# Optimization experiments

Measured on AMD Instinct MI355X. Metric: run time of the kernel, lower is better.

## Reference

```python
import jax, jax.numpy as jnp
import numpy as np

EMB = 512
HEADS = 16
WS = 8          # window size
B = 8
HW = 64         # height = width = sqrt(num_tokens)
N = HW * HW
E_HEAD = EMB // HEADS
WN = HW // WS   # windows per side
SHIFT = WS // 2

# --- static index/mask tables (numpy, baked at trace time) ---
_idx = np.array([[x, y] for x in range(WS) for y in range(WS)])
_REL = _idx[None, :, :] - _idx[:, None, :] + WS - 1   # [WS^2, WS^2, 2]

def _shift_masks():
    m = np.zeros((WS * WS, WS * WS), dtype=np.float32)
    s = WS * (WS // 2)
    m[-s:, :-s] = -np.inf
    m[:-s, -s:] = -np.inf
    r = (WS * WS) // WS
    # einops '(r w1) (c w2) -> (w1 r) (w2 c)'
    col = m.reshape(r, WS, r, WS).transpose(1, 0, 3, 2).reshape(WS * WS, WS * WS)
    return jnp.asarray(m), jnp.asarray(col)

_ROW_MASK, _COL_MASK = _shift_masks()

def _window(x):
    # x: [B, HW, HW, EMB]; channel split '(e H)' -> e outer, H inner
    x = x.reshape(B, WN, WS, WN, WS, E_HEAD, HEADS)
    x = x.transpose(0, 6, 1, 3, 2, 4, 5)            # b H Wh Ww w1 w2 e
    return x.reshape(B, HEADS, WN, WN, WS * WS, E_HEAD)

def _unwindow(x):
    # 'b H Wh Ww (w1 w2) e -> b (Wh w1) (Ww w2) (H e)'
    x = x.reshape(B, HEADS, WN, WN, WS, WS, E_HEAD)
    x = x.transpose(0, 2, 4, 3, 5, 1, 6)
    return x.reshape(B, HW, HW, EMB).reshape(B, N, EMB)

def _forward(content, style, scale, shift,
             W1, b1, W2, b2, Wsc, bsc, Wsh, bsh,
             Wso, bso, Wsho, bsho, pos_emb):
    c = content @ W1.T + b1
    s = style   @ W2.T + b2
    sc = scale  @ Wsc.T + bsc
    sh = shift  @ Wsh.T + bsh
    # to spatial grid and shifted roll (no inverse roll in original code)
    def grid(x):
        x = x.reshape(B, HW, HW, EMB)
        return jnp.roll(x, (-SHIFT, -SHIFT), axis=(1, 2))
    Q  = _window(grid(c))
    K  = _window(grid(s))
    Vs = _window(grid(sc))
    Vh = _window(grid(sh))
    inv_sqrt = 1.0 / np.sqrt(EMB / HEADS)
    wei = jnp.einsum('bhijqe,bhijke->bhijqk', Q, K) * inv_sqrt
    wei = wei + pos_emb[_REL[:, :, 0], _REL[:, :, 1]]
    wei = wei.at[:, :, -1, :].add(_ROW_MASK)
    wei = wei.at[:, :, :, -1].add(_COL_MASK)
    w = jax.nn.softmax(wei, axis=-1)
    out_sc = _unwindow(jnp.einsum('bhijqk,bhijke->bhijqe', w, Vs))
    out_sh = _unwindow(jnp.einsum('bhijqk,bhijke->bhijqe', w, Vh))
    return out_sc @ Wso.T + bso, out_sh @ Wsho.T + bsho

def setup_inputs() -> dict:
    key = jax.random.key(0)
    ks = jax.random.split(key, 18)
    def lin(i):
        return (0.02 * jax.random.normal(ks[i], (EMB, EMB), jnp.float32),
                jnp.zeros((EMB,), jnp.float32))
    W1, b1 = lin(0); W2, b2 = lin(1); Wsc, bsc = lin(2); Wsh, bsh = lin(3)
    Wso, bso = lin(4); Wsho, bsho = lin(5)
    return {
        'content': jax.random.normal(ks[6], (B, N, EMB), jnp.float32),
        'style':   jax.random.normal(ks[7], (B, N, EMB), jnp.float32),
        'scale':   jax.random.normal(ks[8], (B, N, EMB), jnp.float32),
        'shift':   jax.random.normal(ks[9], (B, N, EMB), jnp.float32),
        'W1': W1, 'b1': b1, 'W2': W2, 'b2': b2,
        'Wsc': Wsc, 'bsc': bsc, 'Wsh': Wsh, 'bsh': bsh,
        'Wso': Wso, 'bso': bso, 'Wsho': Wsho, 'bsho': bsho,
        'pos_emb': jax.random.normal(ks[10], (2 * WS - 1, 2 * WS - 1), jnp.float32),
    }

def reference(content, style, scale, shift, W1, b1, W2, b2, Wsc, bsc, Wsh, bsh,
              Wso, bso, Wsho, bsho, pos_emb):
    return _forward(content, style, scale, shift, W1, b1, W2, b2,
                    Wsc, bsc, Wsh, bsh, Wso, bso, Wsho, bsho, pos_emb)
```

## Files before the change

### kernel.cpp

```cpp
#include <hip/hip_runtime.h>
#include <hip/hip_bf16.h>
#include <math.h>

#define EMB 512
#define HEADS 16
#define WS 8
#define BSZ 8
#define HW 64
#define NTOK (HW * HW)
#define WN 8
#define M_TOT (BSZ * NTOK)
#define NELEM ((size_t)M_TOT * EMB)

typedef _Float16 f16;
typedef _Float16 f16x4 __attribute__((ext_vector_type(4)));
typedef _Float16 f16x8 __attribute__((ext_vector_type(8)));
typedef float f32x4 __attribute__((ext_vector_type(4)));

struct CvtW { const float* w[6]; const float* b[4]; f16* out[6]; float* bp; };

__global__ __launch_bounds__(128) void cvt_w(CvtW P) {
  const int z = blockIdx.y;
  const int np = blockIdx.x;
  const int src = (z < 4) ? ((np & 31) * 16 + (np >> 5)) : np;
  const float4* __restrict__ in = (const float4*)(P.w[z] + (size_t)src * 512);
  f16x4* __restrict__ out = (f16x4*)(P.out[z] + (size_t)np * 512);
  const int t = threadIdx.x;
  float4 v = in[t];
  f16x4 h = {(f16)v.x, (f16)v.y, (f16)v.z, (f16)v.w};
  out[t] = h;
  if (t == 0 && z < 4) P.bp[z * 512 + np] = P.b[z][src];
}

struct GemmF16 { const void* X[4]; const f16* W[4]; const float* Bi[4]; void* O[4]; };

template <bool CVT_A, typename OutT>
__global__ __launch_bounds__(256) void gemm_mfma(GemmF16 P) {
  const int z = blockIdx.z;
  const f16* __restrict__ B = P.W[z];
  const float* __restrict__ Bi = P.Bi[z];
  OutT* __restrict__ O = (OutT*)P.O[z];

  __shared__ f16 lds[2][2][128 * 32];

  const int tid = threadIdx.x;
  const int lane = tid & 63;
  const int wid = tid >> 6;
  const int wr = wid >> 1, wc = wid & 1;
  const size_t m0 = (size_t)blockIdx.x * 128;
  const size_t n0 = (size_t)blockIdx.y * 128;

  const f16*  Ag16 = CVT_A ? (const f16*)nullptr : ((const f16*)P.X[z] + m0 * 512);
  const float* Ag32 = CVT_A ? ((const float*)P.X[z] + m0 * 512) : (const float*)nullptr;
  const f16* Bg = B + n0 * 512;

  const int rl = lane >> 2;
  const int qs = (lane & 3) ^ ((rl >> 1) & 3);
  const size_t goff16 = (size_t)rl * 512 + (size_t)qs * 8;

  const int c = lane & 15;
  const int g = lane >> 4;

  int aoff[4], boff[4];
  #pragma unroll
  for (int i = 0; i < 4; ++i) {
    const int rowa = wr * 64 + i * 16 + c;
    aoff[i] = rowa * 32 + ((g ^ ((rowa >> 1) & 3)) * 8);
    const int rowb = wc * 64 + i * 16 + c;
    boff[i] = rowb * 32 + ((g ^ ((rowb >> 1) & 3)) * 8);
  }

  f32x4 acc[4][4];
  #pragma unroll
  for (int i = 0; i < 4; ++i)
    #pragma unroll
    for (int j = 0; j < 4; ++j) acc[i][j] = (f32x4){0.f, 0.f, 0.f, 0.f};

  float4 areg[2][2];

#define LOAD_A32(k0) do { if (CVT_A) {                                         \
    _Pragma("unroll")                                                          \
    for (int ii = 0; ii < 2; ++ii) {                                           \
      const int s = wid * 2 + ii;                                              \
      const float* ga = Ag32 + (size_t)(s * 16 + rl) * 512 + (size_t)(k0)      \
                        + (size_t)qs * 8;                                      \
      areg[ii][0] = *(const float4*)ga;                                        \
      areg[ii][1] = *(const float4*)(ga + 4);                                  \
    } } } while (0)

#define WRITE_A(buf) do { if (CVT_A) {                                         \
    _Pragma("unroll")                                                          \
    for (int ii = 0; ii < 2; ++ii) {                                           \
      const int s = wid * 2 + ii;                                              \
      const float* ap = (const float*)&areg[ii][0];                            \
      f16x8 hv;                                                                \
      _Pragma("unroll")                                                        \
      for (int j = 0; j < 8; ++j) hv[j] = (f16)ap[j];                          \
      *(f16x8*)&lds[buf][0][(size_t)s * 512 + (size_t)lane * 8] = hv;          \
    } } } while (0)

#define STAGE_A16(buf, k0) do { if (!CVT_A) {                                  \
    _Pragma("unroll")                                                          \
    for (int ii = 0; ii < 2; ++ii) {                                           \
      const int s = wid * 2 + ii;                                              \
      const f16* ga = Ag16 + (size_t)s * 16 * 512 + (size_t)(k0) + goff16;     \
      __builtin_amdgcn_global_load_lds(                                        \
          (const __attribute__((address_space(1))) void*)ga,                   \
          (__attribute__((address_space(3))) void*)&lds[buf][0][s * 512],      \
          16, 0, 0);                                                           \
    } } } while (0)

#define STAGE_B(buf, k0) do {                                                  \
    _Pragma("unroll")                                                          \
    for (int ii = 0; ii < 2; ++ii) {                                           \
      const int s = wid * 2 + ii;                                              \
      const f16* gb = Bg + (size_t)s * 16 * 512 + (size_t)(k0) + goff16;       \
      __builtin_amdgcn_global_load_lds(                                        \
          (const __attribute__((address_space(1))) void*)gb,                   \
          (__attribute__((address_space(3))) void*)&lds[buf][1][s * 512],      \
          16, 0, 0);                                                           \
    } } while (0)

  LOAD_A32(0); STAGE_A16(0, 0); STAGE_B(0, 0); WRITE_A(0);
  __syncthreads();

  for (int t = 0; t < 16; ++t) {
    const int cur = t & 1;
    if (t < 15) { LOAD_A32((t + 1) * 32); STAGE_A16(cur ^ 1, (t + 1) * 32);
                  STAGE_B(cur ^ 1, (t + 1) * 32); }
    f16x8 af[4], bf[4];
    #pragma unroll
    for (int i = 0; i < 4; ++i) {
      af[i] = *(const f16x8*)&lds[cur][0][aoff[i]];
      bf[i] = *(const f16x8*)&lds[cur][1][boff[i]];
    }
    #pragma unroll
    for (int mi = 0; mi < 4; ++mi)
      #pragma unroll
      for (int ni = 0; ni < 4; ++ni)
        acc[mi][ni] = __builtin_amdgcn_mfma_f32_16x16x32_f16(
            af[mi], bf[ni], acc[mi][ni], 0, 0, 0);
    if (t < 15) WRITE_A(cur ^ 1);
    __syncthreads();
  }
#undef LOAD_A32
#undef WRITE_A
#undef STAGE_A16
#undef STAGE_B

  const int col_base = (int)n0 + wc * 64;
  const int row_base = (int)m0 + wr * 64 + g * 4;
  float bv[4];
  #pragma unroll
  for (int ni = 0; ni < 4; ++ni) bv[ni] = Bi[col_base + ni * 16 + c];
  #pragma unroll
  for (int mi = 0; mi < 4; ++mi)
    #pragma unroll
    for (int ni = 0; ni < 4; ++ni)
      #pragma unroll
      for (int r = 0; r < 4; ++r) {
        const size_t row = (size_t)(row_base + mi * 16 + r);
        O[row * 512 + col_base + ni * 16 + c] = (OutT)(acc[mi][ni][r] + bv[ni]);
      }
}

__global__ __launch_bounds__(256) void attn_kernel(
    const f16* __restrict__ cq, const f16* __restrict__ ck,
    const f16* __restrict__ vs, const f16* __restrict__ vh,
    const float* __restrict__ pe, f16* __restrict__ osc, f16* __restrict__ osh) {
  __shared__ f16 Pl[4][64][72];
  __shared__ float pesh[228];

  const int tid = threadIdx.x;
  for (int i = tid; i < 225; i += 256) pesh[i] = pe[i];
  __syncthreads();

  const int wid = tid >> 6;
  const int lane = tid & 63;
  const int g = lane >> 4;
  const int c = lane & 15;
  const int w = blockIdx.x * 4 + wid;
  const int wj = w & 7;
  const int wi = (w >> 3) & 7;
  const int h  = (w >> 6) & 15;
  const int b  = w >> 10;

  size_t taddr[4];
  #pragma unroll
  for (int i = 0; i < 4; ++i) {
    const int ty = (wi * 8 + i * 2 + (c >> 3) + 4) & 63;
    const int tx = (wj * 8 + (c & 7) + 4) & 63;
    taddr[i] = ((size_t)b * NTOK + ty * 64 + tx) * EMB + h * 32 + g * 8;
  }
  f16x8 kf[4], qf[4];
  #pragma unroll
  for (int i = 0; i < 4; ++i) {
    kf[i] = *(const f16x8*)(ck + taddr[i]);
    qf[i] = *(const f16x8*)(cq + taddr[i]);
  }

  f32x4 s[4][4];
  #pragma unroll
  for (int mt = 0; mt < 4; ++mt)
    #pragma unroll
    for (int kt = 0; kt < 4; ++kt) s[mt][kt] = (f32x4){0.f, 0.f, 0.f, 0.f};
  #pragma unroll
  for (int mt = 0; mt < 4; ++mt)
    #pragma unroll
    for (int kt = 0; kt < 4; ++kt)
      s[mt][kt] = __builtin_amdgcn_mfma_f32_16x16x32_f16(kf[mt], qf[kt],
                                                         s[mt][kt], 0, 0, 0);

  const float invs = 0.17677669529663687f;
  const bool rm = (wi == 7);
  const bool cm = (wj == 7) && (((c >> 2) & 1) != (g & 1));
  #pragma unroll
  for (int mt = 0; mt < 4; ++mt)
    #pragma unroll
    for (int kt = 0; kt < 4; ++kt) {
      const bool rmask = rm && ((mt >> 1) != (kt >> 1));
      const int ry = (mt - kt) * 2 + (g >> 1) - (c >> 3) + 7;
      #pragma unroll
      for (int r = 0; r < 4; ++r) {
        const int rx = (g & 1) * 4 + r - (c & 7) + 7;
        float d = s[mt][kt][r] * invs + pesh[ry * 15 + rx];
        if (rmask || cm) d = -1e30f;
        s[mt][kt][r] = d;
      }
    }

  #pragma unroll
  for (int kt = 0; kt < 4; ++kt) {
    float m = -1e30f;
    #pragma unroll
    for (int mt = 0; mt < 4; ++mt)
      #pragma unroll
      for (int r = 0; r < 4; ++r) m = fmaxf(m, s[mt][kt][r]);
    m = fmaxf(m, __shfl_xor(m, 16));
    m = fmaxf(m, __shfl_xor(m, 32));
    float sum = 0.f;
    #pragma unroll
    for (int mt = 0; mt < 4; ++mt)
      #pragma unroll
      for (int r = 0; r < 4; ++r) {
        const float p = __expf(s[mt][kt][r] - m);
        s[mt][kt][r] = p;
        sum += p;
      }
    sum += __shfl_xor(sum, 16);
    sum += __shfl_xor(sum, 32);
    const float rs = 1.f / sum;
    #pragma unroll
    for (int mt = 0; mt < 4; ++mt)
      #pragma unroll
      for (int r = 0; r < 4; ++r) s[mt][kt][r] *= rs;
  }

  #pragma unroll
  for (int mt = 0; mt < 4; ++mt)
    #pragma unroll
    for (int kt = 0; kt < 4; ++kt) {
      f16x4 pk = {(f16)s[mt][kt][0], (f16)s[mt][kt][1],
                  (f16)s[mt][kt][2], (f16)s[mt][kt][3]};
      *(f16x4*)&Pl[wid][kt * 16 + c][mt * 16 + g * 4] = pk;
    }

  size_t vb[2];
  #pragma unroll
  for (int ks = 0; ks < 2; ++ks) {
    const int vy = (wi * 8 + ks * 4 + g + 4) & 63;
    vb[ks] = ((size_t)b * NTOK + vy * 64) * EMB + h * 32 + c;
  }
  int xo[8];
  #pragma unroll
  for (int j = 0; j < 8; ++j) xo[j] = ((wj * 8 + j + 4) & 63) * EMB;

  f16x8 vfs[2][2], vfh[2][2];
  #pragma unroll
  for (int nt = 0; nt < 2; ++nt)
    #pragma unroll
    for (int ks = 0; ks < 2; ++ks)
      #pragma unroll
      for (int j = 0; j < 8; ++j) {
        const size_t a = vb[ks] + xo[j] + nt * 16;
        vfs[nt][ks][j] = vs[a];
        vfh[nt][ks][j] = vh[a];
      }

  f16x8 af[4][2];
  #pragma unroll
  for (int mt = 0; mt < 4; ++mt)
    #pragma unroll
    for (int ks = 0; ks < 2; ++ks)
      af[mt][ks] = *(const f16x8*)&Pl[wid][mt * 16 + c][ks * 32 + g * 8];

  size_t ob[4];
  #pragma unroll
  for (int mt = 0; mt < 4; ++mt) {
    const int np = (wi * 8 + 2 * mt + (g >> 1)) * 64 + wj * 8 + 4 * (g & 1);
    ob[mt] = ((size_t)b * NTOK + np) * EMB + h * 32 + c;
  }

  {
    f32x4 o[4][2];
    #pragma unroll
    for (int mt = 0; mt < 4; ++mt)
      #pragma unroll
      for (int nt = 0; nt < 2; ++nt) o[mt][nt] = (f32x4){0.f, 0.f, 0.f, 0.f};
    #pragma unroll
    for (int mt = 0; mt < 4; ++mt)
      #pragma unroll
      for (int nt = 0; nt < 2; ++nt)
        #pragma unroll
        for (int ks = 0; ks < 2; ++ks)
          o[mt][nt] = __builtin_amdgcn_mfma_f32_16x16x32_f16(
              af[mt][ks], vfs[nt][ks], o[mt][nt], 0, 0, 0);
    #pragma unroll
    for (int mt = 0; mt < 4; ++mt)
      #pragma unroll
      for (int nt = 0; nt < 2; ++nt)
        #pragma unroll
        for (int r = 0; r < 4; ++r)
          osc[ob[mt] + (size_t)r * EMB + nt * 16] = (f16)o[mt][nt][r];
  }
  {
    f32x4 o[4][2];
    #pragma unroll
    for (int mt = 0; mt < 4; ++mt)
      #pragma unroll
      for (int nt = 0; nt < 2; ++nt) o[mt][nt] = (f32x4){0.f, 0.f, 0.f, 0.f};
    #pragma unroll
    for (int mt = 0; mt < 4; ++mt)
      #pragma unroll
      for (int nt = 0; nt < 2; ++nt)
        #pragma unroll
        for (int ks = 0; ks < 2; ++ks)
          o[mt][nt] = __builtin_amdgcn_mfma_f32_16x16x32_f16(
              af[mt][ks], vfh[nt][ks], o[mt][nt], 0, 0, 0);
    #pragma unroll
    for (int mt = 0; mt < 4; ++mt)
      #pragma unroll
      for (int nt = 0; nt < 2; ++nt)
        #pragma unroll
        for (int r = 0; r < 4; ++r)
          osh[ob[mt] + (size_t)r * EMB + nt * 16] = (f16)o[mt][nt][r];
  }
}

extern "C" void kernel_launch(void* const* d_in, const int* in_sizes, int n_in,
                              void* d_out, int out_size, void* d_ws, size_t ws_size,
                              hipStream_t stream) {
  const float* content = (const float*)d_in[0];
  const float* style   = (const float*)d_in[1];
  const float* scalex  = (const float*)d_in[2];
  const float* shiftx  = (const float*)d_in[3];
  const float* W1  = (const float*)d_in[4];  const float* b1  = (const float*)d_in[5];
  const float* W2  = (const float*)d_in[6];  const float* b2  = (const float*)d_in[7];
  const float* Wsc = (const float*)d_in[8];  const float* bsc = (const float*)d_in[9];
  const float* Wsh = (const float*)d_in[10]; const float* bsh = (const float*)d_in[11];
  const float* Wso = (const float*)d_in[12]; const float* bso = (const float*)d_in[13];
  const float* Wsho= (const float*)d_in[14]; const float* bsho= (const float*)d_in[15];
  const float* pos = (const float*)d_in[16];
  float* out = (float*)d_out;

  f16* Wh = (f16*)d_ws;
  float* bp = (float*)(Wh + 6 * 262144);
  f16* Ph = (f16*)(bp + 2048);
  f16* Oh = Ph + 4 * NELEM;

  CvtW CW;
  CW.w[0] = W1; CW.w[1] = W2; CW.w[2] = Wsc; CW.w[3] = Wsh; CW.w[4] = Wso; CW.w[5] = Wsho;
  CW.b[0] = b1; CW.b[1] = b2; CW.b[2] = bsc; CW.b[3] = bsh;
  for (int i = 0; i < 6; ++i) CW.out[i] = Wh + (size_t)i * 262144;
  CW.bp = bp;
  hipLaunchKernelGGL(cvt_w, dim3(512, 6), dim3(128), 0, stream, CW);

  GemmF16 P1;
  P1.X[0] = content; P1.X[1] = style; P1.X[2] = scalex; P1.X[3] = shiftx;
  for (int i = 0; i < 4; ++i) {
    P1.W[i] = Wh + (size_t)i * 262144;
    P1.Bi[i] = bp + i * 512;
    P1.O[i] = Ph + (size_t)i * NELEM;
  }
  hipLaunchKernelGGL(HIP_KERNEL_NAME(gemm_mfma<true, f16>),
                     dim3(M_TOT / 128, EMB / 128, 4), dim3(256), 0, stream, P1);

  hipLaunchKernelGGL(attn_kernel, dim3(BSZ * HEADS * WN * WN / 4), dim3(256), 0,
                     stream, Ph, Ph + NELEM, Ph + 2 * NELEM, Ph + 3 * NELEM, pos,
                     Oh, Oh + NELEM);

  GemmF16 P2;
  P2.X[0] = Oh;          P2.W[0] = Wh + 4 * 262144; P2.Bi[0] = bso;  P2.O[0] = out;
  P2.X[1] = Oh + NELEM;  P2.W[1] = Wh + 5 * 262144; P2.Bi[1] = bsho; P2.O[1] = out + NELEM;
  P2.X[2] = P2.X[0]; P2.W[2] = P2.W[0]; P2.Bi[2] = P2.Bi[0]; P2.O[2] = P2.O[0];
  P2.X[3] = P2.X[1]; P2.W[3] = P2.W[1]; P2.Bi[3] = P2.Bi[1]; P2.O[3] = P2.O[1];
  hipLaunchKernelGGL(HIP_KERNEL_NAME(gemm_mfma<false, float>),
                     dim3(M_TOT / 128, EMB / 128, 2), dim3(256), 0, stream, P2);
}
```

Before: 523.7 us.

## Replace LDS-staged GEMM with direct global-to-register MFMA loads and 8 waves

The projection GEMMs no longer stage A and B tiles through shared memory. Each wave now loads its MFMA fragments straight from global memory into registers, using a two-slot register double buffer. Blocks grow to 512 threads (8 waves of 64x32 tiles), which removes the LDS traffic and the per-step barriers. In exchange there is no data sharing inside the block, so global and L2 traffic per block rises, and the per-lane loads are 16-32B strided reads across rows that may coalesce poorly.

```diff
diff --git a/kernel.cpp b/kernel.cpp
--- a/kernel.cpp
+++ b/kernel.cpp
@@ -35,132 +35,105 @@
 struct GemmF16 { const void* X[4]; const f16* W[4]; const float* Bi[4]; void* O[4]; };
 
 template <bool CVT_A, typename OutT>
-__global__ __launch_bounds__(256) void gemm_mfma(GemmF16 P) {
+__global__ __launch_bounds__(512) void gemm_direct(GemmF16 P) {
   const int z = blockIdx.z;
   const f16* __restrict__ B = P.W[z];
   const float* __restrict__ Bi = P.Bi[z];
   OutT* __restrict__ O = (OutT*)P.O[z];
-
-  __shared__ f16 lds[2][2][128 * 32];
+  const float* __restrict__ A32 = CVT_A ? (const float*)P.X[z] : (const float*)nullptr;
+  const f16*  __restrict__ A16 = CVT_A ? (const f16*)nullptr : (const f16*)P.X[z];
 
   const int tid = threadIdx.x;
   const int lane = tid & 63;
   const int wid = tid >> 6;
-  const int wr = wid >> 1, wc = wid & 1;
+  const int wr = wid >> 2;
+  const int wc = wid & 3;
+  const int g = lane >> 4;
+  const int c = lane & 15;
   const size_t m0 = (size_t)blockIdx.x * 128;
   const size_t n0 = (size_t)blockIdx.y * 128;
 
-  const f16*  Ag16 = CVT_A ? (const f16*)nullptr : ((const f16*)P.X[z] + m0 * 512);
-  const float* Ag32 = CVT_A ? ((const float*)P.X[z] + m0 * 512) : (const float*)nullptr;
-  const f16* Bg = B + n0 * 512;
-
-  const int rl = lane >> 2;
-  const int qs = (lane & 3) ^ ((rl >> 1) & 3);
-  const size_t goff16 = (size_t)rl * 512 + (size_t)qs * 8;
-
-  const int c = lane & 15;
-  const int g = lane >> 4;
-
-  int aoff[4], boff[4];
-  #pragma unroll
-  for (int i = 0; i < 4; ++i) {
-    const int rowa = wr * 64 + i * 16 + c;
-    aoff[i] = rowa * 32 + ((g ^ ((rowa >> 1) & 3)) * 8);
-    const int rowb = wc * 64 + i * 16 + c;
-    boff[i] = rowb * 32 + ((g ^ ((rowb >> 1) & 3)) * 8);
-  }
-
-  f32x4 acc[4][4];
-  #pragma unroll
-  for (int i = 0; i < 4; ++i)
-    #pragma unroll
-    for (int j = 0; j < 4; ++j) acc[i][j] = (f32x4){0.f, 0.f, 0.f, 0.f};
-
-  float4 areg[2][2];
-
-#define LOAD_A32(k0) do { if (CVT_A) {                                         \
+  size_t aoff[4], boff[2];
+  #pragma unroll
+  for (int mt = 0; mt < 4; ++mt)
+    aoff[mt] = (m0 + wr * 64 + mt * 16 + c) * 512 + g * 8;
+  #pragma unroll
+  for (int nt = 0; nt < 2; ++nt)
+    boff[nt] = ((size_t)n0 + wc * 32 + nt * 16 + c) * 512 + g * 8;
+
+  f32x4 acc[4][2];
+  #pragma unroll
+  for (int mt = 0; mt < 4; ++mt)
+    #pragma unroll
+    for (int nt = 0; nt < 2; ++nt) acc[mt][nt] = (f32x4){0.f, 0.f, 0.f, 0.f};
+
+  float4 alo0[4], ahi0[4], alo1[4], ahi1[4];
+  f16x8 a0[4], a1[4], b0[2], b1[2];
+
+#define LOADA(SLOT, K0) do {                                                   \
     _Pragma("unroll")                                                          \
-    for (int ii = 0; ii < 2; ++ii) {                                           \
-      const int s = wid * 2 + ii;                                              \
-      const float* ga = Ag32 + (size_t)(s * 16 + rl) * 512 + (size_t)(k0)      \
-                        + (size_t)qs * 8;                                      \
-      areg[ii][0] = *(const float4*)ga;                                        \
-      areg[ii][1] = *(const float4*)(ga + 4);                                  \
-    } } } while (0)
-
-#define WRITE_A(buf) do { if (CVT_A) {                                         \
+    for (int mt = 0; mt < 4; ++mt) {                                           \
+      if (CVT_A) {                                                             \
+        const float* p = A32 + aoff[mt] + (K0);                                \
+        alo##SLOT[mt] = *(const float4*)p;                                     \
+        ahi##SLOT[mt] = *(const float4*)(p + 4);                               \
+      } else {                                                                 \
+        a##SLOT[mt] = *(const f16x8*)(A16 + aoff[mt] + (K0));                  \
+      }                                                                        \
+    } } while (0)
+
+#define LOADB(SLOT, K0) do {                                                   \
     _Pragma("unroll")                                                          \
-    for (int ii = 0; ii < 2; ++ii) {                                           \
-      const int s = wid * 2 + ii;                                              \
-      const float* ap = (const float*)&areg[ii][0];                            \
-      f16x8 hv;                                                                \
+    for (int nt = 0; nt < 2; ++nt)                                             \
+      b##SLOT[nt] = *(const f16x8*)(B + boff[nt] + (K0));                      \
+  } while (0)
+
+#define COMPUTE(SLOT) do {                                                     \
+    f16x8 af[4];                                                               \
+    _Pragma("unroll")                                                          \
+    for (int mt = 0; mt < 4; ++mt) {                                           \
+      if (CVT_A) {                                                             \
+        const float4 u = alo##SLOT[mt], v = ahi##SLOT[mt];                     \
+        f16x8 hv = {(f16)u.x, (f16)u.y, (f16)u.z, (f16)u.w,                    \
+                    (f16)v.x, (f16)v.y, (f16)v.z, (f16)v.w};                   \
+        af[mt] = hv;                                                           \
+      } else {                                                                 \
+        af[mt] = a##SLOT[mt];                                                  \
+      }                                                                        \
+    }                                                                          \
+    _Pragma("unroll")                                                          \
+    for (int mt = 0; mt < 4; ++mt)                                             \
       _Pragma("unroll")                                                        \
-      for (int j = 0; j < 8; ++j) hv[j] = (f16)ap[j];                          \
-      *(f16x8*)&lds[buf][0][(size_t)s * 512 + (size_t)lane * 8] = hv;          \
-    } } } while (0)
-
-#define STAGE_A16(buf, k0) do { if (!CVT_A) {                                  \
-    _Pragma("unroll")                                                          \
-    for (int ii = 0; ii < 2; ++ii) {                                           \
-      const int s = wid * 2 + ii;                                              \
-      const f16* ga = Ag16 + (size_t)s * 16 * 512 + (size_t)(k0) + goff16;     \
-      __builtin_amdgcn_global_load_lds(                                        \
-          (const __attribute__((address_space(1))) void*)ga,                   \
-          (__attribute__((address_space(3))) void*)&lds[buf][0][s * 512],      \
-          16, 0, 0);                                                           \
-    } } } while (0)
-
-#define STAGE_B(buf, k0) do {                                                  \
-    _Pragma("unroll")                                                          \
-    for (int ii = 0; ii < 2; ++ii) {                                           \
-      const int s = wid * 2 + ii;                                              \
-      const f16* gb = Bg + (size_t)s * 16 * 512 + (size_t)(k0) + goff16;       \
-      __builtin_amdgcn_global_load_lds(                                        \
-          (const __attribute__((address_space(1))) void*)gb,                   \
-          (__attribute__((address_space(3))) void*)&lds[buf][1][s * 512],      \
-          16, 0, 0);                                                           \
-    } } while (0)
-
-  LOAD_A32(0); STAGE_A16(0, 0); STAGE_B(0, 0); WRITE_A(0);
-  __syncthreads();
-
-  for (int t = 0; t < 16; ++t) {
-    const int cur = t & 1;
-    if (t < 15) { LOAD_A32((t + 1) * 32); STAGE_A16(cur ^ 1, (t + 1) * 32);
-                  STAGE_B(cur ^ 1, (t + 1) * 32); }
-    f16x8 af[4], bf[4];
-    #pragma unroll
-    for (int i = 0; i < 4; ++i) {
-      af[i] = *(const f16x8*)&lds[cur][0][aoff[i]];
-      bf[i] = *(const f16x8*)&lds[cur][1][boff[i]];
-    }
-    #pragma unroll
-    for (int mi = 0; mi < 4; ++mi)
-      #pragma unroll
-      for (int ni = 0; ni < 4; ++ni)
-        acc[mi][ni] = __builtin_amdgcn_mfma_f32_16x16x32_f16(
-            af[mi], bf[ni], acc[mi][ni], 0, 0, 0);
-    if (t < 15) WRITE_A(cur ^ 1);
-    __syncthreads();
-  }
-#undef LOAD_A32
-#undef WRITE_A
-#undef STAGE_A16
-#undef STAGE_B
-
-  const int col_base = (int)n0 + wc * 64;
+      for (int nt = 0; nt < 2; ++nt)                                           \
+        acc[mt][nt] = __builtin_amdgcn_mfma_f32_16x16x32_f16(                  \
+            af[mt], b##SLOT[nt], acc[mt][nt], 0, 0, 0);                        \
+  } while (0)
+
+  LOADA(0, 0); LOADB(0, 0);
+  #pragma unroll
+  for (int t = 0; t < 16; t += 2) {
+    if (t + 1 < 16) { LOADA(1, (t + 1) * 32); LOADB(1, (t + 1) * 32); }
+    COMPUTE(0);
+    if (t + 2 < 16) { LOADA(0, (t + 2) * 32); LOADB(0, (t + 2) * 32); }
+    if (t + 1 < 16) COMPUTE(1);
+  }
+#undef LOADA
+#undef LOADB
+#undef COMPUTE
+
+  const int col_base = (int)n0 + wc * 32;
   const int row_base = (int)m0 + wr * 64 + g * 4;
-  float bv[4];
-  #pragma unroll
-  for (int ni = 0; ni < 4; ++ni) bv[ni] = Bi[col_base + ni * 16 + c];
-  #pragma unroll
-  for (int mi = 0; mi < 4; ++mi)
-    #pragma unroll
-    for (int ni = 0; ni < 4; ++ni)
+  float bv[2];
+  #pragma unroll
+  for (int nt = 0; nt < 2; ++nt) bv[nt] = Bi[col_base + nt * 16 + c];
+  #pragma unroll
+  for (int mt = 0; mt < 4; ++mt)
+    #pragma unroll
+    for (int nt = 0; nt < 2; ++nt)
       #pragma unroll
       for (int r = 0; r < 4; ++r) {
-        const size_t row = (size_t)(row_base + mi * 16 + r);
-        O[row * 512 + col_base + ni * 16 + c] = (OutT)(acc[mi][ni][r] + bv[ni]);
+        const size_t row = (size_t)(row_base + mt * 16 + r);
+        O[row * 512 + col_base + nt * 16 + c] = (OutT)(acc[mt][nt][r] + bv[nt]);
       }
 }
 
@@ -382,8 +355,8 @@
     P1.Bi[i] = bp + i * 512;
     P1.O[i] = Ph + (size_t)i * NELEM;
   }
-  hipLaunchKernelGGL(HIP_KERNEL_NAME(gemm_mfma<true, f16>),
-                     dim3(M_TOT / 128, EMB / 128, 4), dim3(256), 0, stream, P1);
+  hipLaunchKernelGGL(HIP_KERNEL_NAME(gemm_direct<true, f16>),
+                     dim3(M_TOT / 128, EMB / 128, 4), dim3(512), 0, stream, P1);
 
   hipLaunchKernelGGL(attn_kernel, dim3(BSZ * HEADS * WN * WN / 4), dim3(256), 0,
                      stream, Ph, Ph + NELEM, Ph + 2 * NELEM, Ph + 3 * NELEM, pos,
@@ -394,6 +367,6 @@
   P2.X[1] = Oh + NELEM;  P2.W[1] = Wh + 5 * 262144; P2.Bi[1] = bsho; P2.O[1] = out + NELEM;
   P2.X[2] = P2.X[0]; P2.W[2] = P2.W[0]; P2.Bi[2] = P2.Bi[0]; P2.O[2] = P2.O[0];
   P2.X[3] = P2.X[1]; P2.W[3] = P2.W[1]; P2.Bi[3] = P2.Bi[1]; P2.O[3] = P2.O[1];
-  hipLaunchKernelGGL(HIP_KERNEL_NAME(gemm_mfma<false, float>),
-                     dim3(M_TOT / 128, EMB / 128, 2), dim3(256), 0, stream, P2);
+  hipLaunchKernelGGL(HIP_KERNEL_NAME(gemm_direct<false, float>),
+                     dim3(M_TOT / 128, EMB / 128, 2), dim3(512), 0, stream, P2);
 }
```

Result: slower. 1.047 ms (+100.0%).

## Triple-buffer GEMM LDS staging with explicit vmcnt-based barriers

Applied to the files above, without the earlier changes.

Both projection GEMMs move from double-buffered to triple-buffered LDS staging, prefetching two K-steps ahead. The plain __syncthreads is replaced by inline s_waitcnt vmcnt(N) plus s_barrier, so later async loads can stay in flight across the barrier. The fp32 A path alternates between two register sets so the next load overlaps the convert-and-write. This raises LDS use to 48KB per block and adds register pressure, which may lower occupancy, and correctness depends on the hand-counted vmcnt values matching the number of issued loads.

```diff
diff --git a/kernel.cpp b/kernel.cpp
--- a/kernel.cpp
+++ b/kernel.cpp
@@ -16,6 +16,8 @@
 typedef _Float16 f16x4 __attribute__((ext_vector_type(4)));
 typedef _Float16 f16x8 __attribute__((ext_vector_type(8)));
 typedef float f32x4 __attribute__((ext_vector_type(4)));
+
+#define BAR(N_STR) asm volatile("s_waitcnt vmcnt(" N_STR ") lgkmcnt(0)\n\ts_barrier" ::: "memory")
 
 struct CvtW { const float* w[6]; const float* b[4]; f16* out[6]; float* bp; };
 
@@ -35,13 +37,13 @@
 struct GemmF16 { const void* X[4]; const f16* W[4]; const float* Bi[4]; void* O[4]; };
 
 template <bool CVT_A, typename OutT>
-__global__ __launch_bounds__(256) void gemm_mfma(GemmF16 P) {
+__global__ __launch_bounds__(256) void gemm_pipe(GemmF16 P) {
   const int z = blockIdx.z;
   const f16* __restrict__ B = P.W[z];
   const float* __restrict__ Bi = P.Bi[z];
   OutT* __restrict__ O = (OutT*)P.O[z];
 
-  __shared__ f16 lds[2][2][128 * 32];
+  __shared__ f16 lds[3][2][128 * 32];
 
   const int tid = threadIdx.x;
   const int lane = tid & 63;
@@ -76,23 +78,23 @@
     #pragma unroll
     for (int j = 0; j < 4; ++j) acc[i][j] = (f32x4){0.f, 0.f, 0.f, 0.f};
 
-  float4 areg[2][2];
-
-#define LOAD_A32(k0) do { if (CVT_A) {                                         \
+  float4 alo0[2][2], alo1[2][2];
+
+#define LOAD_A32(SET, k0) do { if (CVT_A) {                                    \
     _Pragma("unroll")                                                          \
     for (int ii = 0; ii < 2; ++ii) {                                           \
       const int s = wid * 2 + ii;                                              \
       const float* ga = Ag32 + (size_t)(s * 16 + rl) * 512 + (size_t)(k0)      \
                         + (size_t)qs * 8;                                      \
-      areg[ii][0] = *(const float4*)ga;                                        \
-      areg[ii][1] = *(const float4*)(ga + 4);                                  \
+      alo##SET[ii][0] = *(const float4*)ga;                                    \
+      alo##SET[ii][1] = *(const float4*)(ga + 4);                              \
     } } } while (0)
 
-#define WRITE_A(buf) do { if (CVT_A) {                                         \
+#define WRITE_A(SET, buf) do { if (CVT_A) {                                    \
     _Pragma("unroll")                                                          \
     for (int ii = 0; ii < 2; ++ii) {                                           \
       const int s = wid * 2 + ii;                                              \
-      const float* ap = (const float*)&areg[ii][0];                            \
+      const float* ap = (const float*)&alo##SET[ii][0];                        \
       f16x8 hv;                                                                \
       _Pragma("unroll")                                                        \
       for (int j = 0; j < 8; ++j) hv[j] = (f16)ap[j];                          \
@@ -121,13 +123,30 @@
           16, 0, 0);                                                           \
     } } while (0)
 
-  LOAD_A32(0); STAGE_A16(0, 0); STAGE_B(0, 0); WRITE_A(0);
-  __syncthreads();
-
+  if (CVT_A) {
+    LOAD_A32(0, 0);  STAGE_B(0, 0);
+    LOAD_A32(1, 32); STAGE_B(1, 32);
+    WRITE_A(0, 0);
+    BAR("6");
+  } else {
+    STAGE_A16(0, 0);  STAGE_B(0, 0);
+    STAGE_A16(1, 32); STAGE_B(1, 32);
+    BAR("4");
+  }
+
+  #pragma unroll
   for (int t = 0; t < 16; ++t) {
-    const int cur = t & 1;
-    if (t < 15) { LOAD_A32((t + 1) * 32); STAGE_A16(cur ^ 1, (t + 1) * 32);
-                  STAGE_B(cur ^ 1, (t + 1) * 32); }
+    const int cur = t % 3;
+    if (t + 2 < 16) {
+      if (CVT_A) {
+        if (((t + 2) & 1) == 0) LOAD_A32(0, (t + 2) * 32);
+        else                    LOAD_A32(1, (t + 2) * 32);
+      } else {
+        STAGE_A16((t + 2) % 3, (t + 2) * 32);
+      }
+      STAGE_B((t + 2) % 3, (t + 2) * 32);
+    }
+
     f16x8 af[4], bf[4];
     #pragma unroll
     for (int i = 0; i < 4; ++i) {
@@ -140,8 +159,18 @@
       for (int ni = 0; ni < 4; ++ni)
         acc[mi][ni] = __builtin_amdgcn_mfma_f32_16x16x32_f16(
             af[mi], bf[ni], acc[mi][ni], 0, 0, 0);
-    if (t < 15) WRITE_A(cur ^ 1);
-    __syncthreads();
+
+    if (CVT_A && t + 1 < 16) {
+      if (((t + 1) & 1) == 0) WRITE_A(0, (t + 1) % 3);
+      else                    WRITE_A(1, (t + 1) % 3);
+    }
+
+    if (t < 14) {
+      if (CVT_A) BAR("6");
+      else       BAR("4");
+    } else if (t == 14) {
+      BAR("0");
+    }
   }
 #undef LOAD_A32
 #undef WRITE_A
@@ -382,7 +411,7 @@
     P1.Bi[i] = bp + i * 512;
     P1.O[i] = Ph + (size_t)i * NELEM;
   }
-  hipLaunchKernelGGL(HIP_KERNEL_NAME(gemm_mfma<true, f16>),
+  hipLaunchKernelGGL(HIP_KERNEL_NAME(gemm_pipe<true, f16>),
                      dim3(M_TOT / 128, EMB / 128, 4), dim3(256), 0, stream, P1);
 
   hipLaunchKernelGGL(attn_kernel, dim3(BSZ * HEADS * WN * WN / 4), dim3(256), 0,
@@ -394,6 +423,6 @@
   P2.X[1] = Oh + NELEM;  P2.W[1] = Wh + 5 * 262144; P2.Bi[1] = bsho; P2.O[1] = out + NELEM;
   P2.X[2] = P2.X[0]; P2.W[2] = P2.W[0]; P2.Bi[2] = P2.Bi[0]; P2.O[2] = P2.O[0];
   P2.X[3] = P2.X[1]; P2.W[3] = P2.W[1]; P2.Bi[3] = P2.Bi[1]; P2.O[3] = P2.O[1];
-  hipLaunchKernelGGL(HIP_KERNEL_NAME(gemm_mfma<false, float>),
+  hipLaunchKernelGGL(HIP_KERNEL_NAME(gemm_pipe<false, float>),
                      dim3(M_TOT / 128, EMB / 128, 2), dim3(256), 0, stream, P2);
 }
```

After: 538.4 us. 2.8% more time.
